# Performance work log

Hardware: AMD Instinct MI355X
Metric: run time of the kernel (lower is better)

The kernel has to match this reference:

```python
import jax, jax.numpy as jnp
import numpy as np

# Fixed architecture constants from Cifar10Model / RetNetConfig
NL = 8            # num_layers
H = 4             # num_heads
D = 64            # hidden_size
QK = 64           # qk_dim
V = 128           # v_dim
QH, VH = QK // H, V // H   # 16, 32 per-head dims
P, IMG, C = 8, 32, 3       # patch size, image size, channels
NP = (IMG // P) ** 2       # 16 patches
T = NP + 1                 # +1 cls token -> 17 tokens
FFN = 12                   # ffn_proj_size


def layer_norm(x, s, b, eps=1e-5):
    mu = x.mean(-1, keepdims=True)
    var = x.var(-1, keepdims=True)
    return (x - mu) * jax.lax.rsqrt(var + eps) * s + b


def rotate_every_two(x):
    x1, x2 = x[..., ::2], x[..., 1::2]
    return jnp.stack([-x2, x1], axis=-1).reshape(x.shape)


def rel_pos(t):
    # xPos-style rotation angles over the per-head qk dim
    angle = 1.0 / (10000 ** jnp.linspace(0.0, 1.0, QH // 2))
    angle = jnp.repeat(angle, 2)                      # (QH,)
    idx = jnp.arange(t, dtype=jnp.float32)[:, None]
    sin, cos = jnp.sin(idx * angle), jnp.cos(idx * angle)   # (t, QH)
    # per-head retention decay gamma (use_default_gamma=False path)
    gamma = 1.0 - jnp.exp(jnp.linspace(np.log(1 / 32), np.log(1 / 512), H))  # (H,)
    n = jnp.arange(t)
    expo = n[:, None] - n[None, :]                    # n - m
    causal = expo >= 0
    dmask = jnp.where(causal, gamma[:, None, None] ** jnp.where(causal, expo, 0), 0.0)  # (H,t,t)
    dmask = dmask / jnp.sqrt(dmask.sum(-1, keepdims=True))   # row-normalized decay
    return sin, cos, dmask


def retention(x, Wq, Wk, Wv, Wg, Wo, sin, cos, dmask):
    b, t, _ = x.shape
    q = (x @ Wq).reshape(b, t, H, QH).transpose(0, 2, 1, 3)   # (b,h,t,qh)
    k = (x @ Wk).reshape(b, t, H, QH).transpose(0, 2, 1, 3)
    v = (x @ Wv).reshape(b, t, H, VH).transpose(0, 2, 1, 3)   # (b,h,t,vh)
    g = x @ Wg                                                # (b,t,V) gate
    q = q * cos + rotate_every_two(q) * sin
    k = (k * cos + rotate_every_two(k) * sin) * (QH ** -0.5)
    scores = jnp.einsum('bhnd,bhmd->bhnm', q, k) * dmask      # decay-masked QK^T
    denom = jnp.clip(jnp.abs(jax.lax.stop_gradient(scores).sum(-1, keepdims=True)), 1.0, None)
    scores = scores / denom                                   # retention row normalization
    o = jnp.einsum('bhnm,bhmd->bhnd', scores, v)              # (b,h,t,vh)
    # per-head group norm (no affine) instead of softmax normalization
    mu = o.mean(-1, keepdims=True)
    var = o.var(-1, keepdims=True)
    o = (o - mu) * jax.lax.rsqrt(var + 1e-5)
    o = o.transpose(0, 2, 1, 3).reshape(b, t, V)
    return (jax.nn.silu(g) * o) @ Wo


def setup_inputs() -> dict:
    key = jax.random.key(0)
    ks = iter(jax.random.split(key, 32))
    s = 0.02
    B = 8192
    inp = {
        'x': jax.random.normal(next(ks), (B, C, IMG, IMG), jnp.float32),
        'patch_w': jax.random.normal(next(ks), (C * P * P, D), jnp.float32) * s,
        'patch_b': jnp.zeros((D,), jnp.float32),
        'cls': jax.random.normal(next(ks), (1, 1, D), jnp.float32) * s,
        'pos': jax.random.normal(next(ks), (T, D), jnp.float32) * s,
        'Wq': jax.random.normal(next(ks), (NL, D, QK), jnp.float32) * s,
        'Wk': jax.random.normal(next(ks), (NL, D, QK), jnp.float32) * s,
        'Wv': jax.random.normal(next(ks), (NL, D, V), jnp.float32) * s,
        'Wg': jax.random.normal(next(ks), (NL, D, V), jnp.float32) * s,
        'Wo': jax.random.normal(next(ks), (NL, V, D), jnp.float32) * s,
        'ln1_s': jnp.ones((NL, D), jnp.float32),
        'ln1_b': jnp.zeros((NL, D), jnp.float32),
        'w1': jax.random.normal(next(ks), (NL, D, FFN), jnp.float32) * s,
        'b1': jnp.zeros((NL, FFN), jnp.float32),
        'w2': jax.random.normal(next(ks), (NL, FFN, D), jnp.float32) * s,
        'b2': jnp.zeros((NL, D), jnp.float32),
        'ln2_s': jnp.ones((NL, D), jnp.float32),
        'ln2_b': jnp.zeros((NL, D), jnp.float32),
        'lnf_s': jnp.ones((D,), jnp.float32),
        'lnf_b': jnp.zeros((D,), jnp.float32),
        'neck_w': jax.random.normal(next(ks), (D, 16), jnp.float32) * s,
        'neck_b': jnp.zeros((16,), jnp.float32),
        'head_w': jax.random.normal(next(ks), (16, 10), jnp.float32) * s,
        'head_b': jnp.zeros((10,), jnp.float32),
    }
    return inp


def reference(x, patch_w, patch_b, cls, pos, Wq, Wk, Wv, Wg, Wo, ln1_s, ln1_b,
              w1, b1, w2, b2, ln2_s, ln2_b, lnf_s, lnf_b, neck_w, neck_b, head_w, head_b):
    b = x.shape[0]
    # patch embedding: stride==kernel conv expressed as reshape + matmul
    xp = x.reshape(b, C, IMG // P, P, IMG // P, P).transpose(0, 2, 4, 1, 3, 5)
    xp = xp.reshape(b, NP, C * P * P)
    tok = xp @ patch_w + patch_b                          # (b,16,64)
    tok = jnp.concatenate([jnp.broadcast_to(cls, (b, 1, D)), tok], axis=1) + pos  # (b,17,64)
    sin, cos, dmask = rel_pos(T)
    h = tok
    for i in range(NL):  # pre-LN RetNet blocks
        h = h + retention(layer_norm(h, ln1_s[i], ln1_b[i]),
                          Wq[i], Wk[i], Wv[i], Wg[i], Wo[i], sin, cos, dmask)
        f = layer_norm(h, ln2_s[i], ln2_b[i])
        h = h + jax.nn.gelu(f @ w1[i] + b1[i]) @ w2[i] + b2[i]
    h = layer_norm(h, lnf_s, lnf_b)
    ys = h[:, -1, :]                                      # last token
    return (ys @ neck_w + neck_b) @ head_w + head_b       # (b,10) logits
```

## Files before the change

kernel.cpp:

```cpp
#include <hip/hip_runtime.h>
#include <hip/hip_bf16.h>

#define NLAY 8
#define MFMA __builtin_amdgcn_mfma_f32_16x16x32_bf16
#define MFMA32 __builtin_amdgcn_mfma_f32_32x32x16_bf16

typedef __attribute__((ext_vector_type(8))) short bf16x8;
typedef __attribute__((ext_vector_type(4))) float f32x4;
typedef __attribute__((ext_vector_type(16))) float f32x16;
typedef __attribute__((ext_vector_type(4))) int i32x4;

template <bool BF16>
__device__ __forceinline__ float ld(const void* p, int i) {
  if (BF16) {
    unsigned short u = ((const unsigned short*)p)[i];
    return __uint_as_float(((unsigned)u) << 16);
  }
  return ((const float*)p)[i];
}

template <bool BF16>
__device__ __forceinline__ float2 ld2(const void* p, int i) {
  float2 r;
  if (BF16) {
    unsigned u = ((const unsigned*)p)[i >> 1];
    r.x = __uint_as_float(u << 16);
    r.y = __uint_as_float(u & 0xffff0000u);
  } else {
    r = ((const float2*)p)[i >> 1];
  }
  return r;
}

__device__ __forceinline__ unsigned pack_bf2(float a, float b) {
  __hip_bfloat16 ha = __float2bfloat16(a), hb = __float2bfloat16(b);
  unsigned short ua, ub;
  __builtin_memcpy(&ua, &ha, 2);
  __builtin_memcpy(&ub, &hb, 2);
  return ((unsigned)ub << 16) | (unsigned)ua;
}

__device__ __forceinline__ unsigned short cvt_bf(float a) {
  __hip_bfloat16 h = __float2bfloat16(a);
  unsigned short us;
  __builtin_memcpy(&us, &h, 2);
  return us;
}

__device__ __forceinline__ float2 unpk(unsigned u) {
  float2 r;
  r.x = __uint_as_float(u << 16);
  r.y = __uint_as_float(u & 0xffff0000u);
  return r;
}

__device__ __forceinline__ bf16x8 as_bf(i32x4 v) {
  bf16x8 r;
  __builtin_memcpy(&r, &v, 16);
  return r;
}

__global__ void setup_tables(float* __restrict__ ws, const void* __restrict__ x) {
  int tid = threadIdx.x;
  for (int idx = tid; idx < 272; idx += 256) {
    int t = idx >> 4, j = idx & 15;
    float a = powf(10000.f, -(float)(j >> 1) / 7.f);
    float arg = (float)t * a;
    ws[idx] = sinf(arg);
    ws[272 + idx] = cosf(arg);
  }
  for (int row = tid; row < 68; row += 256) {
    int hh = row / 17, t = row % 17;
    float gamma = 1.f - exp2f(-5.f - 4.f * (float)hh / 3.f);
    float sum = 0.f;
    for (int u = 0; u <= t; ++u) sum += powf(gamma, (float)(t - u));
    float rn = rsqrtf(sum);
    for (int u = 0; u < 17; ++u)
      ws[544 + row * 17 + u] = (u <= t) ? powf(gamma, (float)(t - u)) * rn : 0.f;
  }
  if (tid == 0) {
    const unsigned short* u16 = (const unsigned short*)x;
    int sane = 0;
    for (int i = 0; i < 128; ++i) {
      float v = __uint_as_float(((unsigned)u16[2 * i]) << 16);
      float av = fabsf(v);
      if (v == 0.f || (av > 1e-8f && av < 1e4f)) sane++;
    }
    ws[1700] = (sane >= 64) ? 1.f : 0.f;
  }
}

#define FRAG_OLD 280576
#define FRAG_TOT 305152
template <bool BF16>
__global__ void prep_frags(const void* __restrict__ patch_w,
                           const void* __restrict__ Wq, const void* __restrict__ Wk,
                           const void* __restrict__ Wv, const void* __restrict__ Wg,
                           const void* __restrict__ Wo, const void* __restrict__ w1,
                           const void* __restrict__ w2,
                           const float* __restrict__ tab,
                           unsigned short* __restrict__ frag) {
  if ((tab[1700] > 0.5f) != BF16) return;
  int g = blockIdx.x * 256 + threadIdx.x;
  if (g >= FRAG_TOT) return;
  float v;
  if (g < 12288) {
    int nt = g / 3072, r = g % 3072, kt = r / 512, r2 = r % 512, la = r2 >> 3, j = r2 & 7;
    int n = nt * 16 + (la & 15), k = kt * 32 + (la >> 4) * 8 + j;
    v = ld<BF16>(patch_w, k * 64 + n);
  } else if (g < FRAG_OLD) {
    int gg = g - 12288, l = gg / 33536, o = gg % 33536;
    if (o < 8192) {
      const void* W = (o < 4096) ? Wq : Wk;
      int e = o & 4095;
      int nt = e / 1024, r = e % 1024, kt = r / 512, r2 = r % 512, la = r2 >> 3, j = r2 & 7;
      int n = nt * 16 + (la & 15), k = kt * 32 + (la >> 4) * 8 + j;
      v = ld<BF16>(W, l * 4096 + k * 64 + n);
    } else if (o < 24576) {
      const void* W = (o < 16384) ? Wv : Wg;
      int e = (o - 8192) & 8191;
      int nt = e / 1024, r = e % 1024, kt = r / 512, r2 = r % 512, la = r2 >> 3, j = r2 & 7;
      int n = nt * 16 + (la & 15), k = kt * 32 + (la >> 4) * 8 + j;
      v = ld<BF16>(W, l * 8192 + k * 128 + n);
    } else if (o < 32768) {
      int e = o - 24576;
      int nt = e / 2048, r = e % 2048, kt = r / 512, r2 = r % 512, la = r2 >> 3, j = r2 & 7;
      int n = nt * 16 + (la & 15), k = kt * 32 + (la >> 4) * 8 + j;
      v = ld<BF16>(Wo, l * 8192 + k * 64 + n);
    } else {
      int e = o - 32768, eo = e / 64, d = e % 64;
      v = ld<BF16>(w1, l * 768 + d * 12 + eo);
    }
  } else {
    int gg = g - FRAG_OLD, l = gg / 3072, o = gg % 3072;
    if (o < 1024) {
      int kt = o >> 9, r = o & 511, la = r >> 3, j = r & 7;
      int n = la & 15, k = kt * 32 + (la >> 4) * 8 + j;
      v = (n < 12) ? ld<BF16>(w1, l * 768 + k * 12 + n) : 0.f;
    } else {
      int e2 = o - 1024;
      int nt = e2 >> 9, r = e2 & 511, la = r >> 3, j = r & 7;
      int n = nt * 16 + (la & 15), k = (la >> 4) * 8 + j;
      v = (k < 12) ? ld<BF16>(w2, (l * 12 + k) * 64 + n) : 0.f;
    }
  }
  __hip_bfloat16 h = __float2bfloat16(v);
  unsigned short us;
  __builtin_memcpy(&us, &h, 2);
  frag[g] = us;
}

#define O_DM   0
#define O_SIN  1156
#define O_COS  1428
#define O_ST   1700
#define O_H    2212
#define O_XNF  4456
#define O_FF   5992
#define O_R    6400
#define O_SCA  11024
#define O_VG   14096
#define SM_TOT 18968

template <bool BF16>
__global__ void __launch_bounds__(512, 4)
vit_fused(const void* __restrict__ x, const void* __restrict__ patch_b,
          const void* __restrict__ cls, const void* __restrict__ pos,
          const void* __restrict__ ln1s, const void* __restrict__ ln1b,
          const void* __restrict__ b1, const void* __restrict__ b2,
          const void* __restrict__ ln2s, const void* __restrict__ ln2b,
          const void* __restrict__ lnfs, const void* __restrict__ lnfb,
          const void* __restrict__ neckw, const void* __restrict__ neckb,
          const void* __restrict__ headw, const void* __restrict__ headb,
          const float* __restrict__ tab, const unsigned short* __restrict__ FR,
          void* __restrict__ out) {
  if ((tab[1700] > 0.5f) != BF16) return;

  const int tid = threadIdx.x;
  const int lane = tid & 63, w = tid >> 6;
  const int lq = lane >> 4, ln = lane & 15;
  const int img0 = 2 * blockIdx.x;

  __shared__ __align__(16) float sm[SM_TOT];
  float* sDM  = sm + O_DM;
  float* sSin = sm + O_SIN;
  float* sCos = sm + O_COS;
  float* sST  = sm + O_ST;
  float* sH   = sm + O_H;
  float* sFF  = sm + O_FF;
  float* sQ   = sm + O_R;
  float* sK   = sm + O_R + 2312;
  float* sO   = sm + O_R;
  float* sSC  = sm + O_SCA;
  unsigned short* sVbT = (unsigned short*)(sm + O_VG);
  unsigned short* sGb  = (unsigned short*)(sm + O_VG) + 5120;
  const bf16x8* FRB = (const bf16x8*)FR;

  for (int i = tid; i < 1156; i += 512) sDM[i] = tab[544 + i] * 0.25f;
  for (int i = tid; i < 272; i += 512) { sSin[i] = tab[i]; sCos[i] = tab[272 + i]; }
  for (int s = tid; s < 768; s += 512) {
    int mt = s / 384, r = s % 384, kt = r / 64, la = r % 64;
    int p = la & 15, q = la >> 4;
    int kb = kt * 32 + q * 8;
    int c = kb >> 6, rem = kb & 63, a = rem >> 3;
    int pi = p >> 2, pj = p & 3;
    int src = (img0 + mt) * 3072 + c * 1024 + (pi * 8 + a) * 32 + pj * 8;
    float v[8];
#pragma unroll
    for (int t2 = 0; t2 < 8; t2 += 2) {
      float2 pv = ld2<BF16>(x, src + t2);
      v[t2] = pv.x; v[t2 + 1] = pv.y;
    }
    i32x4 pk;
    pk.x = pack_bf2(v[0], v[1]); pk.y = pack_bf2(v[2], v[3]);
    pk.z = pack_bf2(v[4], v[5]); pk.w = pack_bf2(v[6], v[7]);
    ((i32x4*)(sm + O_SCA))[s] = pk;
  }
  if (tid < 128) {
    int img = tid >> 6, n = tid & 63;
    sH[(img * 17) * 66 + n] = ld<BF16>(cls, n) + ld<BF16>(pos, n);
  }
  __syncthreads();

  {
    int mt = w >> 2, nt = w & 3;
    f32x4 acc = {0.f, 0.f, 0.f, 0.f};
    const bf16x8* paf = (const bf16x8*)(sm + O_SCA);
#pragma unroll
    for (int kt = 0; kt < 6; ++kt)
      acc = MFMA(paf[(mt * 6 + kt) * 64 + lane], FRB[(nt * 6 + kt) * 64 + lane], acc, 0, 0, 0);
    int n = nt * 16 + ln;
    float pb = ld<BF16>(patch_b, n);
#pragma unroll
    for (int i = 0; i < 4; ++i) {
      int t = 1 + lq * 4 + i;
      sH[(mt * 17 + t) * 66 + n] = acc[i] + pb + ld<BF16>(pos, t * 64 + n);
    }
  }
  __syncthreads();

  for (int l = 0; l < NLAY; ++l) {
    const int LB = 1536 + l * 4192;

    if (tid < 320) {
      int m = tid >> 3, sub = tid & 7;
      i32x4 pk = {0, 0, 0, 0};
      if (m < 34) {
        const float2* hp = (const float2*)(sH + m * 66 + sub * 8);
        float2 h0 = hp[0], h1 = hp[1], h2 = hp[2], h3 = hp[3];
        float s1 = 0.f, s2 = 0.f;
        s1 += h0.x; s2 += h0.x * h0.x; s1 += h0.y; s2 += h0.y * h0.y;
        s1 += h1.x; s2 += h1.x * h1.x; s1 += h1.y; s2 += h1.y * h1.y;
        s1 += h2.x; s2 += h2.x * h2.x; s1 += h2.y; s2 += h2.y * h2.y;
        s1 += h3.x; s2 += h3.x * h3.x; s1 += h3.y; s2 += h3.y * h3.y;
        s1 += __shfl_xor(s1, 1); s2 += __shfl_xor(s2, 1);
        s1 += __shfl_xor(s1, 2); s2 += __shfl_xor(s2, 2);
        s1 += __shfl_xor(s1, 4); s2 += __shfl_xor(s2, 4);
        float mu = s1 * (1.f / 64.f);
        float var = s2 * (1.f / 64.f) - mu * mu;
        float rr = rsqrtf(var + 1e-5f);
        int kb = sub * 8;
        float hv[8] = {h0.x, h0.y, h1.x, h1.y, h2.x, h2.y, h3.x, h3.y};
        float vv[8];
#pragma unroll
        for (int t2 = 0; t2 < 8; t2 += 2) {
          float2 sv = ld2<BF16>(ln1s, l * 64 + kb + t2);
          float2 bv = ld2<BF16>(ln1b, l * 64 + kb + t2);
          vv[t2]     = (hv[t2] - mu) * rr * sv.x + bv.x;
          vv[t2 + 1] = (hv[t2 + 1] - mu) * rr * sv.y + bv.y;
        }
        pk.x = pack_bf2(vv[0], vv[1]); pk.y = pack_bf2(vv[2], vv[3]);
        pk.z = pack_bf2(vv[4], vv[5]); pk.w = pack_bf2(vv[6], vv[7]);
      }
      int slot = (m >> 4) * 128 + (sub >> 2) * 64 + (sub & 3) * 16 + (m & 15);
      ((i32x4*)(sm + O_XNF))[slot] = pk;
    }
    __syncthreads();

    {
      const bf16x8* xnf = (const bf16x8*)(sm + O_XNF);
      {
        const bf16x8* wf = FRB + LB + ((w < 4) ? 0 : 512);
        float* dst = (w < 4) ? sQ : sK;
        int ntl = w & 3;
        int n = ntl * 16 + ln;
#pragma unroll
        for (int mt = 0; mt < 3; ++mt) {
          f32x4 acc = {0.f, 0.f, 0.f, 0.f};
          acc = MFMA(xnf[(mt * 2) * 64 + lane], wf[(ntl * 2) * 64 + lane], acc, 0, 0, 0);
          acc = MFMA(xnf[(mt * 2 + 1) * 64 + lane], wf[(ntl * 2 + 1) * 64 + lane], acc, 0, 0, 0);
          if (mt < 2) {
            float* p = dst + (mt * 16 + lq * 4) * 68 + n;
            p[0] = acc[0]; p[68] = acc[1]; p[136] = acc[2]; p[204] = acc[3];
          } else if (lq == 0) {
            float* p = dst + 32 * 68 + n;
            p[0] = acc[0]; p[68] = acc[1];
          }
        }
      }
      {
        const bf16x8* wf = FRB + LB + 1024;
        int n = w * 16 + ln;
#pragma unroll
        for (int mt = 0; mt < 3; ++mt) {
          f32x4 acc = {0.f, 0.f, 0.f, 0.f};
          acc = MFMA(xnf[(mt * 2) * 64 + lane], wf[(w * 2) * 64 + lane], acc, 0, 0, 0);
          acc = MFMA(xnf[(mt * 2 + 1) * 64 + lane], wf[(w * 2 + 1) * 64 + lane], acc, 0, 0, 0);
          if (mt == 0) {
            uint2 uv;
            uv.x = pack_bf2(acc[0], acc[1]);
            uv.y = pack_bf2(acc[2], acc[3]);
            *(uint2*)(sVbT + n * 20 + lq * 4) = uv;
          } else if (mt == 1) {
#pragma unroll
            for (int i = 0; i < 4; ++i) {
              int m = 16 + lq * 4 + i;
              int img = (m >= 17), t = m - img * 17;
              sVbT[img * 2560 + n * 20 + t] = cvt_bf(acc[i]);
            }
          } else if (lq == 0) {
            sVbT[2560 + n * 20 + 15] = cvt_bf(acc[0]);
            sVbT[2560 + n * 20 + 16] = cvt_bf(acc[1]);
          }
        }
      }
      {
        const bf16x8* wf = FRB + LB + 2048;
        int n = w * 16 + ln;
#pragma unroll
        for (int mt = 0; mt < 3; ++mt) {
          f32x4 acc = {0.f, 0.f, 0.f, 0.f};
          acc = MFMA(xnf[(mt * 2) * 64 + lane], wf[(w * 2) * 64 + lane], acc, 0, 0, 0);
          acc = MFMA(xnf[(mt * 2 + 1) * 64 + lane], wf[(w * 2 + 1) * 64 + lane], acc, 0, 0, 0);
          if (mt < 2) {
            unsigned short* p = sGb + (mt * 16 + lq * 4) * 136 + n;
            p[0] = cvt_bf(acc[0]); p[136] = cvt_bf(acc[1]);
            p[272] = cvt_bf(acc[2]); p[408] = cvt_bf(acc[3]);
          } else if (lq == 0) {
            sGb[32 * 136 + n] = cvt_bf(acc[0]);
            sGb[33 * 136 + n] = cvt_bf(acc[1]);
          }
        }
      }
    }
    __syncthreads();

    {
      int img = w >> 2, hh = w & 3;
      int cl = lane & 31, kh = lane >> 5;
      int tt = (cl < 17) ? cl : 16;
      int rb = (img * 17 + tt) * 68 + hh * 16 + kh * 8;
      int sb = tt * 16 + kh * 8;
      float4 s0 = *(const float4*)(sSin + sb), s1 = *(const float4*)(sSin + sb + 4);
      float4 c0 = *(const float4*)(sCos + sb), c1 = *(const float4*)(sCos + sb + 4);
      float4 qa = *(const float4*)(sQ + rb), qb = *(const float4*)(sQ + rb + 4);
      i32x4 ap;
      ap.x = pack_bf2(qa.x * c0.x - qa.y * s0.x, qa.y * c0.y + qa.x * s0.y);
      ap.y = pack_bf2(qa.z * c0.z - qa.w * s0.z, qa.w * c0.w + qa.z * s0.w);
      ap.z = pack_bf2(qb.x * c1.x - qb.y * s1.x, qb.y * c1.y + qb.x * s1.y);
      ap.w = pack_bf2(qb.z * c1.z - qb.w * s1.z, qb.w * c1.w + qb.z * s1.w);
      float4 ka = *(const float4*)(sK + rb), kb = *(const float4*)(sK + rb + 4);
      i32x4 bp;
      bp.x = pack_bf2(ka.x * c0.x - ka.y * s0.x, ka.y * c0.y + ka.x * s0.y);
      bp.y = pack_bf2(ka.z * c0.z - ka.w * s0.z, ka.w * c0.w + ka.z * s0.w);
      bp.z = pack_bf2(kb.x * c1.x - kb.y * s1.x, kb.y * c1.y + kb.x * s1.y);
      bp.w = pack_bf2(kb.z * c1.z - kb.w * s1.z, kb.w * c1.w + kb.z * s1.w);
      f32x16 acc = {0.f, 0.f, 0.f, 0.f, 0.f, 0.f, 0.f, 0.f,
                    0.f, 0.f, 0.f, 0.f, 0.f, 0.f, 0.f, 0.f};
      acc = MFMA32(as_bf(ap), as_bf(bp), acc, 0, 0, 0);
      if (cl < 17) {
        int scb = img * 1360 + hh * 340;
        const float* dmb = sDM + hh * 289;
#pragma unroll
        for (int r = 0; r < 16; ++r) {
          int t = (r & 3) + 8 * (r >> 2) + 4 * kh;
          if (t < 17) sSC[scb + t * 20 + cl] = acc[r] * dmb[t * 17 + cl];
        }
      }
    }
    __syncthreads();

    {
      int img = w >> 2, hh = w & 3;
      int cl = lane & 31, kh = lane >> 5;
      int tt = (cl < 17) ? cl : 16;
      const float* scb = sSC + img * 1360 + hh * 340;
      const float* rowp = scb + tt * 20;
      float4 p0 = *(const float4*)(rowp);
      float4 p1 = *(const float4*)(rowp + 4);
      float4 p2 = *(const float4*)(rowp + 8);
      float4 p3 = *(const float4*)(rowp + 12);
      float s16v = rowp[16];
      float s = 0.f;
      s += p0.x; s += p0.y; s += p0.z; s += p0.w;
      s += p1.x; s += p1.y; s += p1.z; s += p1.w;
      s += p2.x; s += p2.y; s += p2.z; s += p2.w;
      s += p3.x; s += p3.y; s += p3.z; s += p3.w;
      s += s16v;
      float den = fabsf(s);
      if (den < 1.f) den = 1.f;
      den = 1.f / den;
      float4 av0 = (kh == 0) ? p0 : p2;
      float4 av1 = (kh == 0) ? p1 : p3;
      i32x4 ap;
      ap.x = pack_bf2(av0.x * den, av0.y * den);
      ap.y = pack_bf2(av0.z * den, av0.w * den);
      ap.z = pack_bf2(av1.x * den, av1.y * den);
      ap.w = pack_bf2(av1.z * den, av1.w * den);
      const unsigned short* vcol = sVbT + img * 2560 + (hh * 32 + cl) * 20 + kh * 8;
      const uint2* vq = (const uint2*)vcol;
      uint2 v0 = vq[0], v1 = vq[1];
      i32x4 bp; bp.x = (int)v0.x; bp.y = (int)v0.y; bp.z = (int)v1.x; bp.w = (int)v1.y;
      f32x16 acc = {0.f, 0.f, 0.f, 0.f, 0.f, 0.f, 0.f, 0.f,
                    0.f, 0.f, 0.f, 0.f, 0.f, 0.f, 0.f, 0.f};
      acc = MFMA32(as_bf(ap), as_bf(bp), acc, 0, 0, 0);
      i32x4 a1 = {0, 0, 0, 0}, b1v = {0, 0, 0, 0};
      if (kh == 0) {
        float s16 = s16v * den;
        a1.x = (int)(unsigned)cvt_bf(s16);
        b1v.x = (int)(unsigned)sVbT[img * 2560 + (hh * 32 + cl) * 20 + 16];
      }
      acc = MFMA32(as_bf(a1), as_bf(b1v), acc, 0, 0, 0);
      int cg = hh * 32 + cl;
#pragma unroll
      for (int r = 0; r < 16; ++r) {
        int t = (r & 3) + 8 * (r >> 2) + 4 * kh;
        if (t < 17) sO[(img * 17 + t) * 130 + cg] = acc[r];
      }
    }
    __syncthreads();

    for (int s = tid; s < 768; s += 512) {
      int mt = s >> 8, kt = (s >> 6) & 3, la = s & 63;
      int q = la >> 4, m = mt * 16 + (la & 15);
      int cb = kt * 32 + q * 8;
      i32x4 pk = {0, 0, 0, 0};
      if (m < 34) {
        const float2* op = (const float2*)(sO + m * 130 + cb);
        float2 o0 = op[0], o1 = op[1], o2 = op[2], o3 = op[3];
        float s1 = 0.f, s2 = 0.f;
        s1 += o0.x; s2 += o0.x * o0.x; s1 += o0.y; s2 += o0.y * o0.y;
        s1 += o1.x; s2 += o1.x * o1.x; s1 += o1.y; s2 += o1.y * o1.y;
        s1 += o2.x; s2 += o2.x * o2.x; s1 += o2.y; s2 += o2.y * o2.y;
        s1 += o3.x; s2 += o3.x * o3.x; s1 += o3.y; s2 += o3.y * o3.y;
        s1 += __shfl_xor(s1, 16); s2 += __shfl_xor(s2, 16);
        s1 += __shfl_xor(s1, 32); s2 += __shfl_xor(s2, 32);
        float mu = s1 * (1.f / 32.f);
        float var = s2 * (1.f / 32.f) - mu * mu;
        float rr = rsqrtf(var + 1e-5f);
        i32x4 gu = *(const i32x4*)(sGb + m * 136 + cb);
        float ov[8] = {o0.x, o0.y, o1.x, o1.y, o2.x, o2.y, o3.x, o3.y};
        float vv[8];
#pragma unroll
        for (int q2 = 0; q2 < 4; ++q2) {
          unsigned gw = (q2 == 0) ? (unsigned)gu.x : (q2 == 1) ? (unsigned)gu.y
                       : (q2 == 2) ? (unsigned)gu.z : (unsigned)gu.w;
          float2 gv = unpk(gw);
          float on0 = (ov[2 * q2] - mu) * rr;
          float on1 = (ov[2 * q2 + 1] - mu) * rr;
          vv[2 * q2]     = on0 * (gv.x / (1.f + __expf(-gv.x)));
          vv[2 * q2 + 1] = on1 * (gv.y / (1.f + __expf(-gv.y)));
        }
        pk.x = pack_bf2(vv[0], vv[1]); pk.y = pack_bf2(vv[2], vv[3]);
        pk.z = pack_bf2(vv[4], vv[5]); pk.w = pack_bf2(vv[6], vv[7]);
      }
      ((i32x4*)(sm + O_SCA))[s] = pk;
    }
    __syncthreads();

    {
      const bf16x8* oaf = (const bf16x8*)(sm + O_SCA);
      const bf16x8* wof = FRB + LB + 3072;
      for (int j = w; j < 12; j += 8) {
        int mt = j >> 2, nt = j & 3;
        f32x4 acc = {0.f, 0.f, 0.f, 0.f};
#pragma unroll
        for (int kt = 0; kt < 4; ++kt)
          acc = MFMA(oaf[(mt * 4 + kt) * 64 + lane], wof[(nt * 4 + kt) * 64 + lane], acc, 0, 0, 0);
        int n = nt * 16 + ln;
#pragma unroll
        for (int i = 0; i < 4; ++i) {
          int m = mt * 16 + lq * 4 + i;
          if (m < 34) sH[m * 66 + n] += acc[i];
        }
      }
    }
    __syncthreads();

    if (tid < 320) {
      int m = tid >> 3, sub = tid & 7;
      i32x4 pk = {0, 0, 0, 0};
      if (m < 34) {
        const float2* hp = (const float2*)(sH + m * 66 + sub * 8);
        float2 h0 = hp[0], h1 = hp[1], h2 = hp[2], h3 = hp[3];
        float s1 = 0.f, s2 = 0.f;
        s1 += h0.x; s2 += h0.x * h0.x; s1 += h0.y; s2 += h0.y * h0.y;
        s1 += h1.x; s2 += h1.x * h1.x; s1 += h1.y; s2 += h1.y * h1.y;
        s1 += h2.x; s2 += h2.x * h2.x; s1 += h2.y; s2 += h2.y * h2.y;
        s1 += h3.x; s2 += h3.x * h3.x; s1 += h3.y; s2 += h3.y * h3.y;
        s1 += __shfl_xor(s1, 1); s2 += __shfl_xor(s2, 1);
        s1 += __shfl_xor(s1, 2); s2 += __shfl_xor(s2, 2);
        s1 += __shfl_xor(s1, 4); s2 += __shfl_xor(s2, 4);
        float mu = s1 * (1.f / 64.f);
        float var = s2 * (1.f / 64.f) - mu * mu;
        float rr = rsqrtf(var + 1e-5f);
        int kb = sub * 8;
        float hv[8] = {h0.x, h0.y, h1.x, h1.y, h2.x, h2.y, h3.x, h3.y};
        float vv[8];
#pragma unroll
        for (int t2 = 0; t2 < 8; t2 += 2) {
          float2 sv = ld2<BF16>(ln2s, l * 64 + kb + t2);
          float2 bv = ld2<BF16>(ln2b, l * 64 + kb + t2);
          vv[t2]     = (hv[t2] - mu) * rr * sv.x + bv.x;
          vv[t2 + 1] = (hv[t2 + 1] - mu) * rr * sv.y + bv.y;
        }
        pk.x = pack_bf2(vv[0], vv[1]); pk.y = pack_bf2(vv[2], vv[3]);
        pk.z = pack_bf2(vv[4], vv[5]); pk.w = pack_bf2(vv[6], vv[7]);
      }
      int slot = (m >> 4) * 128 + (sub >> 2) * 64 + (sub & 3) * 16 + (m & 15);
      ((i32x4*)(sm + O_XNF))[slot] = pk;
    }
    __syncthreads();

    if (w < 3) {
      const bf16x8* xnf = (const bf16x8*)(sm + O_XNF);
      const bf16x8* w1f = FRB + 35072 + l * 384;
      int mt = w;
      f32x4 acc = {0.f, 0.f, 0.f, 0.f};
#pragma unroll
      for (int kt = 0; kt < 2; ++kt)
        acc = MFMA(xnf[(mt * 2 + kt) * 64 + lane], w1f[kt * 64 + lane], acc, 0, 0, 0);
      if (ln < 12) {
        float b = ld<BF16>(b1, l * 12 + ln);
#pragma unroll
        for (int i = 0; i < 4; ++i) {
          int m = mt * 16 + lq * 4 + i;
          if (m < 34) {
            float a = acc[i] + b;
            float inner = 0.7978845608028654f * (a + 0.044715f * a * a * a);
            float e = __expf(2.f * inner);
            float th = 1.f - 2.f / (e + 1.f);
            sFF[m * 12 + ln] = 0.5f * a * (1.f + th);
          }
        }
      }
    }
    __syncthreads();

    {
      const bf16x8* w2f = FRB + 35072 + l * 384 + 128;
      for (int j = w; j < 12; j += 8) {
        int mt = j >> 2, nt = j & 3;
        i32x4 ap = {0, 0, 0, 0};
        int ma = mt * 16 + ln;
        if (ma < 34) {
          const float* fp = sFF + ma * 12;
          if (lq == 0) {
            ap.x = pack_bf2(fp[0], fp[1]); ap.y = pack_bf2(fp[2], fp[3]);
            ap.z = pack_bf2(fp[4], fp[5]); ap.w = pack_bf2(fp[6], fp[7]);
          } else if (lq == 1) {
            ap.x = pack_bf2(fp[8], fp[9]); ap.y = pack_bf2(fp[10], fp[11]);
          }
        }
        f32x4 acc = {0.f, 0.f, 0.f, 0.f};
        acc = MFMA(as_bf(ap), w2f[nt * 64 + lane], acc, 0, 0, 0);
        int n = nt * 16 + ln;
        float b = ld<BF16>(b2, l * 64 + n);
#pragma unroll
        for (int i = 0; i < 4; ++i) {
          int m = mt * 16 + lq * 4 + i;
          if (m < 34) sH[m * 66 + n] += acc[i] + b;
        }
      }
    }
    __syncthreads();
  }

  if (tid < 2) {
    int m = tid * 17 + 16;
    float s1 = 0.f, s2 = 0.f;
    for (int d = 0; d < 64; ++d) {
      float v = sH[m * 66 + d];
      s1 += v; s2 += v * v;
    }
    float mu = s1 * (1.f / 64.f);
    float var = s2 * (1.f / 64.f) - mu * mu;
    sST[tid] = mu;
    sST[2 + tid] = rsqrtf(var + 1e-5f);
  }
  __syncthreads();
  if (tid < 32) {
    int img = tid >> 4, jn = tid & 15;
    int m = img * 17 + 16;
    float mu = sST[img], rr = sST[2 + img];
    float acc = ld<BF16>(neckb, jn);
    for (int d = 0; d < 64; ++d) {
      float yn = (sH[m * 66 + d] - mu) * rr * ld<BF16>(lnfs, d) + ld<BF16>(lnfb, d);
      acc += yn * ld<BF16>(neckw, d * 16 + jn);
    }
    sST[8 + img * 16 + jn] = acc;
  }
  __syncthreads();
  if (tid < 20) {
    int img = tid / 10, o = tid % 10;
    float acc = ld<BF16>(headb, o);
#pragma unroll
    for (int e = 0; e < 16; ++e) acc += sST[8 + img * 16 + e] * ld<BF16>(headw, e * 10 + o);
    if (BF16) {
      ((__hip_bfloat16*)out)[(img0 + img) * 10 + o] = __float2bfloat16(acc);
    } else {
      ((float*)out)[(img0 + img) * 10 + o] = acc;
    }
  }
}

extern "C" void kernel_launch(void* const* d_in, const int* in_sizes, int n_in,
                              void* d_out, int out_size, void* d_ws, size_t ws_size,
                              hipStream_t stream) {
  float* tab = (float*)d_ws;
  unsigned short* frag = (unsigned short*)((char*)d_ws + 8192);

  setup_tables<<<dim3(1), dim3(256), 0, stream>>>(tab, d_in[0]);

  const int prepBlocks = (FRAG_TOT + 255) / 256;
  prep_frags<false><<<dim3(prepBlocks), dim3(256), 0, stream>>>(
      d_in[1], d_in[5], d_in[6], d_in[7], d_in[8], d_in[9], d_in[12], d_in[14], tab, frag);
  prep_frags<true><<<dim3(prepBlocks), dim3(256), 0, stream>>>(
      d_in[1], d_in[5], d_in[6], d_in[7], d_in[8], d_in[9], d_in[12], d_in[14], tab, frag);

  const int B = in_sizes[0] / 3072;
  const int grid = B / 2;

  vit_fused<false><<<dim3(grid), dim3(512), 0, stream>>>(
      d_in[0], d_in[2], d_in[3], d_in[4], d_in[10], d_in[11], d_in[13],
      d_in[15], d_in[16], d_in[17], d_in[18], d_in[19], d_in[20], d_in[21],
      d_in[22], d_in[23], tab, frag, d_out);
  vit_fused<true><<<dim3(grid), dim3(512), 0, stream>>>(
      d_in[0], d_in[2], d_in[3], d_in[4], d_in[10], d_in[11], d_in[13],
      d_in[15], d_in[16], d_in[17], d_in[18], d_in[19], d_in[20], d_in[21],
      d_in[22], d_in[23], tab, frag, d_out);
}
```

Measured before the change: 791.1 us.

## Keep retention scores in registers and fuse score normalization into PV MFMA

```diff
diff --git a/kernel.cpp b/kernel.cpp
--- a/kernel.cpp
+++ b/kernel.cpp
@@ -191,7 +191,6 @@
   float* sQ   = sm + O_R;
   float* sK   = sm + O_R + 2312;
   float* sO   = sm + O_R;
-  float* sSC  = sm + O_SCA;
   unsigned short* sVbT = (unsigned short*)(sm + O_VG);
   unsigned short* sGb  = (unsigned short*)(sm + O_VG) + 5120;
   const bf16x8* FRB = (const bf16x8*)FR;
@@ -243,7 +242,9 @@
     const int LB = 1536 + l * 4192;
 
     if (tid < 320) {
-      int m = tid >> 3, sub = tid & 7;
+      int la = tid & 63, wv = tid >> 6;
+      int m = wv * 8 + (la & 7);
+      int sub = ((la >> 3) & 3) + 4 * (la >> 5);
       i32x4 pk = {0, 0, 0, 0};
       if (m < 34) {
         const float2* hp = (const float2*)(sH + m * 66 + sub * 8);
@@ -253,9 +254,9 @@
         s1 += h1.x; s2 += h1.x * h1.x; s1 += h1.y; s2 += h1.y * h1.y;
         s1 += h2.x; s2 += h2.x * h2.x; s1 += h2.y; s2 += h2.y * h2.y;
         s1 += h3.x; s2 += h3.x * h3.x; s1 += h3.y; s2 += h3.y * h3.y;
-        s1 += __shfl_xor(s1, 1); s2 += __shfl_xor(s2, 1);
-        s1 += __shfl_xor(s1, 2); s2 += __shfl_xor(s2, 2);
-        s1 += __shfl_xor(s1, 4); s2 += __shfl_xor(s2, 4);
+        s1 += __shfl_xor(s1, 8);  s2 += __shfl_xor(s2, 8);
+        s1 += __shfl_xor(s1, 16); s2 += __shfl_xor(s2, 16);
+        s1 += __shfl_xor(s1, 32); s2 += __shfl_xor(s2, 32);
         float mu = s1 * (1.f / 64.f);
         float var = s2 * (1.f / 64.f) - mu * mu;
         float rr = rsqrtf(var + 1e-5f);
@@ -365,67 +366,55 @@
       bp.y = pack_bf2(ka.z * c0.z - ka.w * s0.z, ka.w * c0.w + ka.z * s0.w);
       bp.z = pack_bf2(kb.x * c1.x - kb.y * s1.x, kb.y * c1.y + kb.x * s1.y);
       bp.w = pack_bf2(kb.z * c1.z - kb.w * s1.z, kb.w * c1.w + kb.z * s1.w);
+      const unsigned short* vcol = sVbT + img * 2560 + (hh * 32 + cl) * 20 + kh * 8;
+      uint2 v0 = ((const uint2*)vcol)[0], v1 = ((const uint2*)vcol)[1];
+      i32x4 bpv; bpv.x = (int)v0.x; bpv.y = (int)v0.y; bpv.z = (int)v1.x; bpv.w = (int)v1.y;
+      unsigned short v16 = sVbT[img * 2560 + (hh * 32 + cl) * 20 + 16];
+      __syncthreads();
+
       f32x16 acc = {0.f, 0.f, 0.f, 0.f, 0.f, 0.f, 0.f, 0.f,
                     0.f, 0.f, 0.f, 0.f, 0.f, 0.f, 0.f, 0.f};
-      acc = MFMA32(as_bf(ap), as_bf(bp), acc, 0, 0, 0);
-      if (cl < 17) {
-        int scb = img * 1360 + hh * 340;
-        const float* dmb = sDM + hh * 289;
-#pragma unroll
-        for (int r = 0; r < 16; ++r) {
-          int t = (r & 3) + 8 * (r >> 2) + 4 * kh;
-          if (t < 17) sSC[scb + t * 20 + cl] = acc[r] * dmb[t * 17 + cl];
-        }
-      }
-    }
-    __syncthreads();
-
-    {
-      int img = w >> 2, hh = w & 3;
-      int cl = lane & 31, kh = lane >> 5;
-      int tt = (cl < 17) ? cl : 16;
-      const float* scb = sSC + img * 1360 + hh * 340;
-      const float* rowp = scb + tt * 20;
-      float4 p0 = *(const float4*)(rowp);
-      float4 p1 = *(const float4*)(rowp + 4);
-      float4 p2 = *(const float4*)(rowp + 8);
-      float4 p3 = *(const float4*)(rowp + 12);
-      float s16v = rowp[16];
-      float s = 0.f;
-      s += p0.x; s += p0.y; s += p0.z; s += p0.w;
-      s += p1.x; s += p1.y; s += p1.z; s += p1.w;
-      s += p2.x; s += p2.y; s += p2.z; s += p2.w;
-      s += p3.x; s += p3.y; s += p3.z; s += p3.w;
-      s += s16v;
-      float den = fabsf(s);
+      acc = MFMA32(as_bf(bp), as_bf(ap), acc, 0, 0, 0);
+      const float* dmr = sDM + hh * 289 + tt * 17;
+      float p[16];
+#pragma unroll
+      for (int r = 0; r < 16; ++r) {
+        int u = (r & 3) + 8 * (r >> 2) + 4 * kh;
+        p[r] = (u <= 16) ? acc[r] * dmr[u] : 0.f;
+      }
+      float own = 0.f;
+#pragma unroll
+      for (int r = 0; r < 16; ++r) own += p[r];
+      float den = fabsf(own + __shfl_xor(own, 32));
       if (den < 1.f) den = 1.f;
       den = 1.f / den;
-      float4 av0 = (kh == 0) ? p0 : p2;
-      float4 av1 = (kh == 0) ? p1 : p3;
-      i32x4 ap;
-      ap.x = pack_bf2(av0.x * den, av0.y * den);
-      ap.y = pack_bf2(av0.z * den, av0.w * den);
-      ap.z = pack_bf2(av1.x * den, av1.y * den);
-      ap.w = pack_bf2(av1.z * den, av1.w * den);
-      const unsigned short* vcol = sVbT + img * 2560 + (hh * 32 + cl) * 20 + kh * 8;
-      const uint2* vq = (const uint2*)vcol;
-      uint2 v0 = vq[0], v1 = vq[1];
-      i32x4 bp; bp.x = (int)v0.x; bp.y = (int)v0.y; bp.z = (int)v1.x; bp.w = (int)v1.y;
-      f32x16 acc = {0.f, 0.f, 0.f, 0.f, 0.f, 0.f, 0.f, 0.f,
-                    0.f, 0.f, 0.f, 0.f, 0.f, 0.f, 0.f, 0.f};
-      acc = MFMA32(as_bf(ap), as_bf(bp), acc, 0, 0, 0);
+      float ex[4];
+#pragma unroll
+      for (int j = 0; j < 4; ++j)
+        ex[j] = __shfl_xor((kh == 0) ? p[4 + j] : p[j], 32);
+      float pd[8];
+#pragma unroll
+      for (int j = 0; j < 4; ++j) {
+        pd[j]     = ((kh == 0) ? p[j]  : ex[j])     * den;
+        pd[4 + j] = ((kh == 0) ? ex[j] : p[4 + j])  * den;
+      }
+      i32x4 apv;
+      apv.x = pack_bf2(pd[0], pd[1]); apv.y = pack_bf2(pd[2], pd[3]);
+      apv.z = pack_bf2(pd[4], pd[5]); apv.w = pack_bf2(pd[6], pd[7]);
+      f32x16 ao = {0.f, 0.f, 0.f, 0.f, 0.f, 0.f, 0.f, 0.f,
+                   0.f, 0.f, 0.f, 0.f, 0.f, 0.f, 0.f, 0.f};
+      ao = MFMA32(as_bf(apv), as_bf(bpv), ao, 0, 0, 0);
       i32x4 a1 = {0, 0, 0, 0}, b1v = {0, 0, 0, 0};
       if (kh == 0) {
-        float s16 = s16v * den;
-        a1.x = (int)(unsigned)cvt_bf(s16);
-        b1v.x = (int)(unsigned)sVbT[img * 2560 + (hh * 32 + cl) * 20 + 16];
-      }
-      acc = MFMA32(as_bf(a1), as_bf(b1v), acc, 0, 0, 0);
+        a1.x = (int)(unsigned)cvt_bf(p[8] * den);
+        b1v.x = (int)(unsigned)v16;
+      }
+      ao = MFMA32(as_bf(a1), as_bf(b1v), ao, 0, 0, 0);
       int cg = hh * 32 + cl;
 #pragma unroll
       for (int r = 0; r < 16; ++r) {
         int t = (r & 3) + 8 * (r >> 2) + 4 * kh;
-        if (t < 17) sO[(img * 17 + t) * 130 + cg] = acc[r];
+        if (t < 17) sO[(img * 17 + t) * 134 + cg] = ao[r];
       }
     }
     __syncthreads();
@@ -436,7 +425,7 @@
       int cb = kt * 32 + q * 8;
       i32x4 pk = {0, 0, 0, 0};
       if (m < 34) {
-        const float2* op = (const float2*)(sO + m * 130 + cb);
+        const float2* op = (const float2*)(sO + m * 134 + cb);
         float2 o0 = op[0], o1 = op[1], o2 = op[2], o3 = op[3];
         float s1 = 0.f, s2 = 0.f;
         s1 += o0.x; s2 += o0.x * o0.x; s1 += o0.y; s2 += o0.y * o0.y;
@@ -488,7 +477,9 @@
     __syncthreads();
 
     if (tid < 320) {
-      int m = tid >> 3, sub = tid & 7;
+      int la = tid & 63, wv = tid >> 6;
+      int m = wv * 8 + (la & 7);
+      int sub = ((la >> 3) & 3) + 4 * (la >> 5);
       i32x4 pk = {0, 0, 0, 0};
       if (m < 34) {
         const float2* hp = (const float2*)(sH + m * 66 + sub * 8);
@@ -498,9 +489,9 @@
         s1 += h1.x; s2 += h1.x * h1.x; s1 += h1.y; s2 += h1.y * h1.y;
         s1 += h2.x; s2 += h2.x * h2.x; s1 += h2.y; s2 += h2.y * h2.y;
         s1 += h3.x; s2 += h3.x * h3.x; s1 += h3.y; s2 += h3.y * h3.y;
-        s1 += __shfl_xor(s1, 1); s2 += __shfl_xor(s2, 1);
-        s1 += __shfl_xor(s1, 2); s2 += __shfl_xor(s2, 2);
-        s1 += __shfl_xor(s1, 4); s2 += __shfl_xor(s2, 4);
+        s1 += __shfl_xor(s1, 8);  s2 += __shfl_xor(s2, 8);
+        s1 += __shfl_xor(s1, 16); s2 += __shfl_xor(s2, 16);
+        s1 += __shfl_xor(s1, 32); s2 += __shfl_xor(s2, 32);
         float mu = s1 * (1.f / 64.f);
         float var = s2 * (1.f / 64.f) - mu * mu;
         float rr = rsqrtf(var + 1e-5f);
```

After: 762.7 us. 3.6% less time.
